# Kernel optimization log

Hardware: AMD Instinct MI355X
Metric: run time of the kernel (lower is better)

## Reference

```python
import jax, jax.numpy as jnp
import numpy as np
import math

N = 262144   # number of voxels (MHA batch dim, batch_first=True)
T = 1        # tgt_len (one query per voxel)
S = 9        # src_len (9 shifted-grid neighbors)
E = 32       # embed_dim
H = 2        # num_heads
HD = E // H  # head_dim = 16
SIGMA = 10.0 # hardcoded in gauss_MultiheadAttention.__init__


def setup_inputs() -> dict:
    key0 = jax.random.key(0)
    ks = jax.random.split(key0, 8)
    query = jax.random.normal(ks[0], (N, T, E), dtype=jnp.float32)
    key_t = jax.random.normal(ks[1], (N, S, E), dtype=jnp.float32)
    value = jax.random.normal(ks[2], (N, S, E), dtype=jnp.float32)
    gauss = jax.random.uniform(ks[3], (N, S), dtype=jnp.float32)  # nonneg squared-distance-like
    # packed in-projection weight [3E, E] (xavier_uniform) and zero bias, as in _reset_parameters
    limit = math.sqrt(6.0 / (3 * E + E))
    in_proj_weight = jax.random.uniform(ks[4], (3 * E, E), dtype=jnp.float32, minval=-limit, maxval=limit)
    in_proj_bias = jnp.zeros((3 * E,), dtype=jnp.float32)
    lim_o = math.sqrt(1.0 / E)
    out_proj_weight = jax.random.uniform(ks[5], (E, E), dtype=jnp.float32, minval=-lim_o, maxval=lim_o)
    out_proj_bias = jnp.zeros((E,), dtype=jnp.float32)
    return {
        "query": query, "key": key_t, "value": value, "gauss": gauss,
        "in_proj_weight": in_proj_weight, "in_proj_bias": in_proj_bias,
        "out_proj_weight": out_proj_weight, "out_proj_bias": out_proj_bias,
    }


def reference(query, key, value, gauss, in_proj_weight, in_proj_bias,
              out_proj_weight, out_proj_bias):
    # q/k/v in-projection (packed weight chunked in 3, q is not k so chunk path)
    w_q, w_k, w_v = in_proj_weight[:E], in_proj_weight[E:2 * E], in_proj_weight[2 * E:]
    b_q, b_k, b_v = in_proj_bias[:E], in_proj_bias[E:2 * E], in_proj_bias[2 * E:]
    q = jnp.einsum('bte,fe->btf', query, w_q) + b_q   # [N,T,E]
    k = jnp.einsum('bse,fe->bsf', key, w_k) + b_k     # [N,S,E]
    v = jnp.einsum('bse,fe->bsf', value, w_v) + b_v   # [N,S,E]
    # split heads: [N, len, H, HD] -> [N, H, len, HD]
    q = q.reshape(N, T, H, HD).transpose(0, 2, 1, 3)
    k = k.reshape(N, S, H, HD).transpose(0, 2, 1, 3)
    v = v.reshape(N, S, H, HD).transpose(0, 2, 1, 3)
    # scaled dot product; scale by sqrt(head_dim) (E in the kernel = per-head dim)
    q = q / math.sqrt(HD)
    attn = jnp.einsum('bhtd,bhsd->bhts', q, k)        # [N,H,T,S]
    # multiplicative gaussian reweighting applied to every head (even+odd rows)
    gauss_weight = jnp.exp(-gauss * SIGMA)[:, None, None, :]  # [N,1,1,S]
    attn = attn * gauss_weight
    attn = jax.nn.softmax(attn, axis=-1)
    # dropout_p=0 (eval-mode reference; dropout is stochastic)
    out = jnp.einsum('bhts,bhsd->bhtd', attn, v)      # [N,H,T,HD]
    out = out.transpose(0, 2, 1, 3).reshape(N, T, E)  # merge heads
    out = jnp.einsum('bte,fe->btf', out, out_proj_weight) + out_proj_bias
    return out
```

## Files before the change

### kernel.cpp

```cpp
#include <hip/hip_runtime.h>
#include <math.h>

#define SS 9
#define EE 32
#define TPB 256

#define WS_M0   0
#define WS_PT0  2048
#define WS_UB   4096
#define WS_U    4160
#define WS_BO2  4224
#define WS_C    4256

__global__ void gauss_prep_kernel(const float* __restrict__ ipw,
                                  const float* __restrict__ ipb,
                                  const float* __restrict__ opw,
                                  const float* __restrict__ opb,
                                  float* __restrict__ dw) {
  const int tid = threadIdx.x;
  for (int idx = tid; idx < 2048; idx += TPB) {
    const int h = idx >> 10, e = (idx >> 5) & 31, e2 = idx & 31;
    float acc = 0.f;
    for (int d = 0; d < 16; ++d)
      acc += ipw[(h * 16 + d) * 32 + e] * ipw[(32 + h * 16 + d) * 32 + e2];
    dw[WS_M0 + idx] = 0.25f * acc;
  }
  for (int idx = tid; idx < 2048; idx += TPB) {
    const int h = idx >> 10, e = (idx >> 5) & 31, f = idx & 31;
    float acc = 0.f;
    for (int d = 0; d < 16; ++d)
      acc += opw[f * 32 + h * 16 + d] * ipw[(64 + h * 16 + d) * 32 + e];
    dw[WS_PT0 + idx] = acc;
  }
  if (tid < 64) {
    const int h = tid >> 5, e = tid & 31;
    float a_ub = 0.f, a_u = 0.f;
    for (int d = 0; d < 16; ++d) {
      a_ub += ipb[h * 16 + d] * ipw[(32 + h * 16 + d) * 32 + e];
      a_u  += ipw[(h * 16 + d) * 32 + e] * ipb[32 + h * 16 + d];
    }
    dw[WS_UB + tid] = 0.25f * a_ub;
    dw[WS_U + tid]  = 0.25f * a_u;
  } else if (tid < 96) {
    const int f = tid - 64;
    float acc = opb[f];
    for (int j = 0; j < 32; ++j) acc += ipb[64 + j] * opw[f * 32 + j];
    dw[WS_BO2 + f] = acc;
  } else if (tid < 98) {
    const int h = tid - 96;
    float acc = 0.f;
    for (int d = 0; d < 16; ++d) acc += ipb[h * 16 + d] * ipb[32 + h * 16 + d];
    dw[WS_C + h] = 0.25f * acc;
  }
}

__global__ __launch_bounds__(TPB) void gauss_attn_kernel(
    const float* __restrict__ query,
    const float* __restrict__ key,
    const float* __restrict__ value,
    const float* __restrict__ gauss,
    const float* __restrict__ dw,
    float* __restrict__ out) {
  const int tid = threadIdx.x;
  const long b = (long)blockIdx.x * TPB + tid;

  float qreg[32];
  {
    const float4* qp = (const float4*)(query + b * EE);
    #pragma unroll
    for (int i = 0; i < 8; ++i) {
      const float4 v = qp[i];
      qreg[4 * i] = v.x; qreg[4 * i + 1] = v.y;
      qreg[4 * i + 2] = v.z; qreg[4 * i + 3] = v.w;
    }
  }
  float gw[SS];
  {
    const float* gp = gauss + b * SS;
    #pragma unroll
    for (int s = 0; s < SS; ++s) gw[s] = gp[s];
  }

  float t00 = dw[WS_C + 0], t01 = dw[WS_C + 1];
  #pragma unroll
  for (int e = 0; e < 32; ++e) {
    t00 += qreg[e] * dw[WS_U + e];
    t01 += qreg[e] * dw[WS_U + 32 + e];
  }

  float wv0[32], wv1[32];
  #pragma unroll
  for (int e2 = 0; e2 < 32; ++e2) {
    wv0[e2] = dw[WS_UB + e2];
    wv1[e2] = dw[WS_UB + 32 + e2];
  }
  #pragma unroll
  for (int e = 0; e < 32; ++e) {
    const float qe = qreg[e];
    #pragma unroll
    for (int e2 = 0; e2 < 32; ++e2) {
      wv0[e2] += qe * dw[WS_M0 + e * 32 + e2];
      wv1[e2] += qe * dw[WS_M0 + 1024 + e * 32 + e2];
    }
  }

  #pragma unroll
  for (int s = 0; s < SS; ++s) gw[s] = __expf(-10.0f * gw[s]);

  float qk0[SS], qk1[SS];
  {
    const float4* kp = (const float4*)(key + b * (long)(SS * EE));
    #pragma unroll
    for (int s = 0; s < SS; ++s) {
      float a0 = t00, a1 = t01;
      #pragma unroll
      for (int j = 0; j < 8; ++j) {
        const float4 v = kp[s * 8 + j];
        a0 += wv0[4*j]*v.x + wv0[4*j+1]*v.y + wv0[4*j+2]*v.z + wv0[4*j+3]*v.w;
        a1 += wv1[4*j]*v.x + wv1[4*j+1]*v.y + wv1[4*j+2]*v.z + wv1[4*j+3]*v.w;
      }
      qk0[s] = a0; qk1[s] = a1;
    }
  }

  float p0[SS], p1[SS];
  {
    float m0 = -1e30f, m1 = -1e30f;
    #pragma unroll
    for (int s = 0; s < SS; ++s) {
      qk0[s] *= gw[s]; qk1[s] *= gw[s];
      m0 = fmaxf(m0, qk0[s]); m1 = fmaxf(m1, qk1[s]);
    }
    float l0 = 0.f, l1 = 0.f;
    #pragma unroll
    for (int s = 0; s < SS; ++s) {
      p0[s] = __expf(qk0[s] - m0); l0 += p0[s];
      p1[s] = __expf(qk1[s] - m1); l1 += p1[s];
    }
    const float r0 = 1.f / l0, r1 = 1.f / l1;
    #pragma unroll
    for (int s = 0; s < SS; ++s) { p0[s] *= r0; p1[s] *= r1; }
  }

  float vb0[32], vb1[32];
  #pragma unroll
  for (int e = 0; e < 32; ++e) { vb0[e] = 0.f; vb1[e] = 0.f; }
  {
    const float4* vp = (const float4*)(value + b * (long)(SS * EE));
    #pragma unroll
    for (int s = 0; s < SS; ++s) {
      const float w0 = p0[s], w1 = p1[s];
      #pragma unroll
      for (int j = 0; j < 8; ++j) {
        const float4 v = vp[s * 8 + j];
        vb0[4*j]   += w0 * v.x; vb0[4*j+1] += w0 * v.y;
        vb0[4*j+2] += w0 * v.z; vb0[4*j+3] += w0 * v.w;
        vb1[4*j]   += w1 * v.x; vb1[4*j+1] += w1 * v.y;
        vb1[4*j+2] += w1 * v.z; vb1[4*j+3] += w1 * v.w;
      }
    }
  }

  float o[32];
  #pragma unroll
  for (int f = 0; f < 32; ++f) o[f] = dw[WS_BO2 + f];
  #pragma unroll
  for (int e = 0; e < 32; ++e) {
    const float x0 = vb0[e], x1 = vb1[e];
    #pragma unroll
    for (int f = 0; f < 32; ++f) {
      o[f] += x0 * dw[WS_PT0 + e * 32 + f];
      o[f] += x1 * dw[WS_PT0 + 1024 + e * 32 + f];
    }
  }

  {
    float4* op = (float4*)(out + b * EE);
    #pragma unroll
    for (int i = 0; i < 8; ++i)
      op[i] = make_float4(o[4*i], o[4*i+1], o[4*i+2], o[4*i+3]);
  }
}

extern "C" void kernel_launch(void* const* d_in, const int* in_sizes, int n_in,
                              void* d_out, int out_size, void* d_ws, size_t ws_size,
                              hipStream_t stream) {
  const float* query = (const float*)d_in[0];
  const float* key   = (const float*)d_in[1];
  const float* value = (const float*)d_in[2];
  const float* gauss = (const float*)d_in[3];
  const float* ipw   = (const float*)d_in[4];
  const float* ipb   = (const float*)d_in[5];
  const float* opw   = (const float*)d_in[6];
  const float* opb   = (const float*)d_in[7];
  float* out = (float*)d_out;
  float* dw  = (float*)d_ws;

  const int n = in_sizes[0] / EE;
  gauss_prep_kernel<<<1, TPB, 0, stream>>>(ipw, ipb, opw, opb, dw);
  gauss_attn_kernel<<<n / TPB, TPB, 0, stream>>>(query, key, value, gauss, dw, out);
}
```

Measured before the change: 677.4 us.

## Stage key/value rows through double-buffered LDS with async global_load_lds

The attention kernel now uses 64-thread blocks. Global loads of query, key and value go through global_load_lds into double-buffered, XOR-swizzled shared memory, so each wave issues coalesced 16-byte loads across the 8 rows in a group instead of strided per-thread row reads. The next key or value slice is prefetched while the current one is consumed, with explicit vmcnt waits. This targets uncoalesced per-thread loads and exposed memory latency. In exchange it adds LDS traffic, relies on hand-written waitcnt counting, and lowers threads per block.

Result: slower. 1.877 ms (+177.1%).

```diff
diff --git a/kernel.cpp b/kernel.cpp
--- a/kernel.cpp
+++ b/kernel.cpp
@@ -3,7 +3,8 @@
 
 #define SS 9
 #define EE 32
-#define TPB 256
+#define PTPB 256
+#define ATPB 64
 
 #define WS_M0   0
 #define WS_PT0  2048
@@ -18,14 +19,14 @@
                                   const float* __restrict__ opb,
                                   float* __restrict__ dw) {
   const int tid = threadIdx.x;
-  for (int idx = tid; idx < 2048; idx += TPB) {
+  for (int idx = tid; idx < 2048; idx += PTPB) {
     const int h = idx >> 10, e = (idx >> 5) & 31, e2 = idx & 31;
     float acc = 0.f;
     for (int d = 0; d < 16; ++d)
       acc += ipw[(h * 16 + d) * 32 + e] * ipw[(32 + h * 16 + d) * 32 + e2];
     dw[WS_M0 + idx] = 0.25f * acc;
   }
-  for (int idx = tid; idx < 2048; idx += TPB) {
+  for (int idx = tid; idx < 2048; idx += PTPB) {
     const int h = idx >> 10, e = (idx >> 5) & 31, f = idx & 31;
     float acc = 0.f;
     for (int d = 0; d < 16; ++d)
@@ -54,32 +55,52 @@
   }
 }
 
-__global__ __launch_bounds__(TPB) void gauss_attn_kernel(
+__device__ __forceinline__ void load16(const float* g, float4* l) {
+  __builtin_amdgcn_global_load_lds(
+      (const __attribute__((address_space(1))) void*)g,
+      (__attribute__((address_space(3))) void*)l, 16, 0, 0);
+}
+
+__global__ __launch_bounds__(ATPB, 2) void gauss_attn_kernel(
     const float* __restrict__ query,
     const float* __restrict__ key,
     const float* __restrict__ value,
     const float* __restrict__ gauss,
     const float* __restrict__ dw,
     float* __restrict__ out) {
-  const int tid = threadIdx.x;
-  const long b = (long)blockIdx.x * TPB + tid;
-
-  float qreg[32];
-  {
-    const float4* qp = (const float4*)(query + b * EE);
-    #pragma unroll
-    for (int i = 0; i < 8; ++i) {
-      const float4 v = qp[i];
-      qreg[4 * i] = v.x; qreg[4 * i + 1] = v.y;
-      qreg[4 * i + 2] = v.z; qreg[4 * i + 3] = v.w;
-    }
-  }
+  __shared__ float4 kt[2][512];
+
+  const int l = threadIdx.x;
+  const int g = l >> 3;
+  const int c = l & 7;
+  const int sw = c ^ g;
+  const long rb = (long)blockIdx.x * ATPB;
+
+  const float* qs   = query + (rb + g) * EE + sw * 4;
+  const float* ks   = key   + (rb + g) * (long)(SS * EE) + sw * 4;
+  const float* vsrc = value + (rb + g) * (long)(SS * EE) + sw * 4;
+
   float gw[SS];
   {
-    const float* gp = gauss + b * SS;
+    const float* gp = gauss + (rb + l) * SS;
     #pragma unroll
     for (int s = 0; s < SS; ++s) gw[s] = gp[s];
   }
+
+  #pragma unroll
+  for (int i = 0; i < 8; ++i) load16(qs + i * (8 * EE), &kt[0][i * 64]);
+  #pragma unroll
+  for (int i = 0; i < 8; ++i) load16(ks + i * (8 * SS * EE), &kt[1][i * 64]);
+
+  asm volatile("s_waitcnt vmcnt(8)" ::: "memory");
+  float qreg[32];
+  #pragma unroll
+  for (int j = 0; j < 8; ++j) {
+    const float4 v = kt[0][(l << 3) | (j ^ c)];
+    qreg[4*j] = v.x; qreg[4*j+1] = v.y; qreg[4*j+2] = v.z; qreg[4*j+3] = v.w;
+  }
+  #pragma unroll
+  for (int i = 0; i < 8; ++i) load16(ks + EE + i * (8 * SS * EE), &kt[0][i * 64]);
 
   float t00 = dw[WS_C + 0], t01 = dw[WS_C + 1];
   #pragma unroll
@@ -87,7 +108,6 @@
     t00 += qreg[e] * dw[WS_U + e];
     t01 += qreg[e] * dw[WS_U + 32 + e];
   }
-
   float wv0[32], wv1[32];
   #pragma unroll
   for (int e2 = 0; e2 < 32; ++e2) {
@@ -103,23 +123,33 @@
       wv1[e2] += qe * dw[WS_M0 + 1024 + e * 32 + e2];
     }
   }
-
   #pragma unroll
   for (int s = 0; s < SS; ++s) gw[s] = __expf(-10.0f * gw[s]);
 
   float qk0[SS], qk1[SS];
-  {
-    const float4* kp = (const float4*)(key + b * (long)(SS * EE));
-    #pragma unroll
-    for (int s = 0; s < SS; ++s) {
-      float a0 = t00, a1 = t01;
+  #pragma unroll
+  for (int s = 0; s < SS; ++s) {
+    const int b = (s + 1) & 1;
+    asm volatile("s_waitcnt vmcnt(8)" ::: "memory");
+    float4 ch[8];
+    #pragma unroll
+    for (int j = 0; j < 8; ++j) ch[j] = kt[b][(l << 3) | (j ^ c)];
+    float a0 = t00, a1 = t01;
+    #pragma unroll
+    for (int j = 0; j < 8; ++j) {
+      a0 += wv0[4*j]*ch[j].x + wv0[4*j+1]*ch[j].y + wv0[4*j+2]*ch[j].z + wv0[4*j+3]*ch[j].w;
+      a1 += wv1[4*j]*ch[j].x + wv1[4*j+1]*ch[j].y + wv1[4*j+2]*ch[j].z + wv1[4*j+3]*ch[j].w;
+    }
+    qk0[s] = a0 * gw[s]; qk1[s] = a1 * gw[s];
+    if (s + 2 <= SS - 1) {
       #pragma unroll
-      for (int j = 0; j < 8; ++j) {
-        const float4 v = kp[s * 8 + j];
-        a0 += wv0[4*j]*v.x + wv0[4*j+1]*v.y + wv0[4*j+2]*v.z + wv0[4*j+3]*v.w;
-        a1 += wv1[4*j]*v.x + wv1[4*j+1]*v.y + wv1[4*j+2]*v.z + wv1[4*j+3]*v.w;
-      }
-      qk0[s] = a0; qk1[s] = a1;
+      for (int i = 0; i < 8; ++i)
+        load16(ks + (s + 2) * EE + i * (8 * SS * EE), &kt[b][i * 64]);
+    } else {
+      const int v2 = s + 2 - SS;
+      #pragma unroll
+      for (int i = 0; i < 8; ++i)
+        load16(vsrc + v2 * EE + i * (8 * SS * EE), &kt[b][i * 64]);
     }
   }
 
@@ -128,7 +158,6 @@
     float m0 = -1e30f, m1 = -1e30f;
     #pragma unroll
     for (int s = 0; s < SS; ++s) {
-      qk0[s] *= gw[s]; qk1[s] *= gw[s];
       m0 = fmaxf(m0, qk0[s]); m1 = fmaxf(m1, qk1[s]);
     }
     float l0 = 0.f, l1 = 0.f;
@@ -145,19 +174,26 @@
   float vb0[32], vb1[32];
   #pragma unroll
   for (int e = 0; e < 32; ++e) { vb0[e] = 0.f; vb1[e] = 0.f; }
-  {
-    const float4* vp = (const float4*)(value + b * (long)(SS * EE));
-    #pragma unroll
-    for (int s = 0; s < SS; ++s) {
-      const float w0 = p0[s], w1 = p1[s];
+  #pragma unroll
+  for (int s = 0; s < SS; ++s) {
+    const int b = s & 1;
+    if (s == SS - 1) asm volatile("s_waitcnt vmcnt(0)" ::: "memory");
+    else             asm volatile("s_waitcnt vmcnt(8)" ::: "memory");
+    float4 ch[8];
+    #pragma unroll
+    for (int j = 0; j < 8; ++j) ch[j] = kt[b][(l << 3) | (j ^ c)];
+    const float w0 = p0[s], w1 = p1[s];
+    #pragma unroll
+    for (int j = 0; j < 8; ++j) {
+      vb0[4*j]   += w0 * ch[j].x; vb0[4*j+1] += w0 * ch[j].y;
+      vb0[4*j+2] += w0 * ch[j].z; vb0[4*j+3] += w0 * ch[j].w;
+      vb1[4*j]   += w1 * ch[j].x; vb1[4*j+1] += w1 * ch[j].y;
+      vb1[4*j+2] += w1 * ch[j].z; vb1[4*j+3] += w1 * ch[j].w;
+    }
+    if (s + 2 < SS) {
       #pragma unroll
-      for (int j = 0; j < 8; ++j) {
-        const float4 v = vp[s * 8 + j];
-        vb0[4*j]   += w0 * v.x; vb0[4*j+1] += w0 * v.y;
-        vb0[4*j+2] += w0 * v.z; vb0[4*j+3] += w0 * v.w;
-        vb1[4*j]   += w1 * v.x; vb1[4*j+1] += w1 * v.y;
-        vb1[4*j+2] += w1 * v.z; vb1[4*j+3] += w1 * v.w;
-      }
+      for (int i = 0; i < 8; ++i)
+        load16(vsrc + (s + 2) * EE + i * (8 * SS * EE), &kt[b][i * 64]);
     }
   }
 
@@ -175,7 +211,7 @@
   }
 
   {
-    float4* op = (float4*)(out + b * EE);
+    float4* op = (float4*)(out + (rb + l) * EE);
     #pragma unroll
     for (int i = 0; i < 8; ++i)
       op[i] = make_float4(o[4*i], o[4*i+1], o[4*i+2], o[4*i+3]);
@@ -197,6 +233,6 @@
   float* dw  = (float*)d_ws;
 
   const int n = in_sizes[0] / EE;
-  gauss_prep_kernel<<<1, TPB, 0, stream>>>(ipw, ipb, opw, opb, dw);
-  gauss_attn_kernel<<<n / TPB, TPB, 0, stream>>>(query, key, value, gauss, dw, out);
-}
+  gauss_prep_kernel<<<1, PTPB, 0, stream>>>(ipw, ipb, opw, opb, dw);
+  gauss_attn_kernel<<<n / ATPB, ATPB, 0, stream>>>(query, key, value, gauss, dw, out);
+}
```
